# Performance work log

Hardware: AMD Instinct MI355X
Metric: run time of the kernel (lower is better)

Reference implementation:

```python
import jax, jax.numpy as jnp
import numpy as np

HIDDEN = 1024
NUM_HEADS = 16
HEAD_DIM = HIDDEN // NUM_HEADS
WINDOW = 512


def setup_inputs() -> dict:
    key = jax.random.key(0)
    ks = jax.random.split(key, 6)
    b, s = 2, 4096
    x = jax.random.normal(ks[0], (b, s, HIDDEN), dtype=jnp.float32)
    attention_mask = jnp.ones((b, s), dtype=jnp.int32)
    scale = 1.0 / np.sqrt(HIDDEN)
    Wq = jax.random.normal(ks[1], (HIDDEN, HIDDEN), dtype=jnp.float32) * scale
    Wk = jax.random.normal(ks[2], (HIDDEN, HIDDEN), dtype=jnp.float32) * scale
    Wv = jax.random.normal(ks[3], (HIDDEN, HIDDEN), dtype=jnp.float32) * scale
    Wo = jax.random.normal(ks[4], (HIDDEN, HIDDEN), dtype=jnp.float32) * scale
    return {"x": x, "attention_mask": attention_mask,
            "Wq": Wq, "Wk": Wk, "Wv": Wv, "Wo": Wo}


def reference(x, attention_mask, Wq, Wk, Wv, Wo):
    b, s, d = x.shape
    # nn.Linear computes x @ W.T
    q = (x @ Wq.T).reshape(b, s, NUM_HEADS, HEAD_DIM).transpose(0, 2, 1, 3)
    k = (x @ Wk.T).reshape(b, s, NUM_HEADS, HEAD_DIM).transpose(0, 2, 1, 3)
    v = (x @ Wv.T).reshape(b, s, NUM_HEADS, HEAD_DIM).transpose(0, 2, 1, 3)
    # [b,h,s,s] scores
    scores = jnp.einsum('bhqd,bhkd->bhqk', q, k) / np.sqrt(HEAD_DIM)
    # causal sliding-window mask: allow j <= i and j >= i - window + 1
    i = jnp.arange(s)[:, None]
    j = jnp.arange(s)[None, :]
    window_mask = (j <= i) & (j >= i - WINDOW + 1)  # [s,s]
    neg_inf = jnp.finfo(scores.dtype).min
    scores = jnp.where(window_mask[None, None], scores, neg_inf)
    pad = attention_mask.astype(bool)[:, None, None, :]  # [b,1,1,s]
    scores = jnp.where(pad, scores, neg_inf)
    probs = jax.nn.softmax(scores, axis=-1)
    out = jnp.einsum('bhqk,bhkd->bhqd', probs, v)
    out = out.transpose(0, 2, 1, 3).reshape(b, s, d)
    return out @ Wo.T
```

## Files before the change

### kernel.cpp

```cpp
#include <hip/hip_runtime.h>
#include <cstdint>
#include <cstddef>

#define HID 1024
#define SEQ 4096
#define NB  2
#define NH  16
#define HD  64
#define WIN 512
#define TOK (NB*SEQ)

typedef _Float16 f16x8 __attribute__((ext_vector_type(8)));
typedef _Float16 f16x4 __attribute__((ext_vector_type(4)));
typedef float    f32x4 __attribute__((ext_vector_type(4)));

__global__ __launch_bounds__(256)
void convert_kernel(const float* __restrict__ X, const float* __restrict__ w0,
                    const float* __restrict__ w1, const float* __restrict__ w2,
                    const float* __restrict__ w3,
                    _Float16* __restrict__ Xh, _Float16* __restrict__ Wh) {
  const int bi = blockIdx.x;
  const float* src; _Float16* dst; size_t off;
  if (bi < 4096) {
    src = X; dst = Xh; off = (size_t)bi * 2048;
  } else {
    const int wi = bi - 4096, z = wi >> 9;
    src = (z == 0) ? w0 : (z == 1) ? w1 : (z == 2) ? w2 : w3;
    dst = Wh + (size_t)z * HID * HID;
    off = (size_t)(wi & 511) * 2048;
  }
  const size_t i = off + (size_t)threadIdx.x * 8;
  f32x4 a = *(const f32x4*)(src + i);
  f32x4 b = *(const f32x4*)(src + i + 4);
  f16x8 o;
#pragma unroll
  for (int r = 0; r < 4; ++r) { o[r] = (_Float16)a[r]; o[r+4] = (_Float16)b[r]; }
  *(f16x8*)(dst + i) = o;
}

__device__ __forceinline__ void gload16(const void* g, void* lds) {
  __builtin_amdgcn_global_load_lds(
      (__attribute__((address_space(1))) void*)(void*)g,
      (__attribute__((address_space(3))) void*)lds, 16, 0, 0);
}

__device__ __forceinline__ void gemm_mainloop(
    const _Float16* __restrict__ A, const _Float16* __restrict__ W,
    _Float16* sA, _Float16* sB, f32x4 (&acc)[4][4], int m0, int n0) {
  const int tid  = threadIdx.x;
  const int lane = tid & 63;
  const int wave = tid >> 6;
  const int wm = wave >> 1, wn = wave & 1;
  const int l15 = lane & 15, quad = lane >> 4;

  const int o0 = tid * 16;
  const int o1 = o0 + 4096;
  const _Float16* a0 = A + (size_t)(m0 + (o0 >> 6)) * HID + ((o0 & 63) >> 1);
  const _Float16* a1 = A + (size_t)(m0 + (o1 >> 6)) * HID + ((o1 & 63) >> 1);
  const _Float16* w0 = W + (size_t)(n0 + (o0 >> 6)) * HID + ((o0 & 63) >> 1);
  const _Float16* w1 = W + (size_t)(n0 + (o1 >> 6)) * HID + ((o1 & 63) >> 1);
  _Float16* la0 = sA + (o0 >> 1);
  _Float16* la1 = sA + (o1 >> 1);
  _Float16* lb0 = sB + (o0 >> 1);
  _Float16* lb1 = sB + (o1 >> 1);

  const int aoff = (wm*64 + l15)*32 + quad*8;
  const int boff = (wn*64 + l15)*32 + quad*8;

  for (int k0 = 0; k0 < HID; k0 += 64) {
    __syncthreads();
    gload16(a0 + k0,      la0);
    gload16(a1 + k0,      la1);
    gload16(a0 + k0 + 32, la0 + 4096);
    gload16(a1 + k0 + 32, la1 + 4096);
    gload16(w0 + k0,      lb0);
    gload16(w1 + k0,      lb1);
    gload16(w0 + k0 + 32, lb0 + 4096);
    gload16(w1 + k0 + 32, lb1 + 4096);
    __syncthreads();
#pragma unroll
    for (int s = 0; s < 2; ++s) {
      const int sb = s * 4096;
      f16x8 af[4], wf[4];
#pragma unroll
      for (int t = 0; t < 4; ++t) {
        af[t] = *(const f16x8*)(sA + sb + aoff + t*512);
        wf[t] = *(const f16x8*)(sB + sb + boff + t*512);
      }
#pragma unroll
      for (int i = 0; i < 4; ++i)
#pragma unroll
        for (int j = 0; j < 4; ++j)
          acc[i][j] = __builtin_amdgcn_mfma_f32_16x16x32_f16(af[i], wf[j], acc[i][j], 0, 0, 0);
    }
  }
}

__global__ __launch_bounds__(256, 3)
void gemm_qkv_kernel(const _Float16* __restrict__ X,
                     const _Float16* __restrict__ Wh,
                     _Float16* __restrict__ Q,
                     _Float16* __restrict__ Kb,
                     _Float16* __restrict__ Vt) {
  __shared__ __align__(16) _Float16 sA[128*64];
  __shared__ __align__(16) _Float16 sB[128*64];
  const int i  = blockIdx.x;
  const int g  = i & 7;
  const int j  = i >> 3;
  const int mi = j & 7;
  const int c  = j >> 3;
  const int z  = c >> 3;
  const int n0 = (c & 7) * 128;
  const int m0 = (g*8 + mi) * 128;
  const _Float16* W = Wh + (size_t)z * HID * HID;
  f32x4 acc[4][4] = {};
  gemm_mainloop(X, W, sA, sB, acc, m0, n0);

  const int tid  = threadIdx.x;
  const int lane = tid & 63;
  const int wave = tid >> 6;
  const int wm = wave >> 1, wn = wave & 1;
  const int l15 = lane & 15, quad = lane >> 4;

  if (z < 2) {
    _Float16* C = (z == 0) ? Q : Kb;
    const float scl = (z == 0) ? 0.125f : 1.0f;
#pragma unroll
    for (int tm = 0; tm < 4; ++tm)
#pragma unroll
      for (int tn = 0; tn < 4; ++tn) {
        const int row = m0 + wm*64 + tm*16 + quad*4;
        const int col = n0 + wn*64 + tn*16 + l15;
#pragma unroll
        for (int r = 0; r < 4; ++r)
          C[(size_t)(row + r)*HID + col] = (_Float16)(acc[tm][tn][r] * scl);
      }
  } else {
#pragma unroll
    for (int tm = 0; tm < 4; ++tm)
#pragma unroll
      for (int tn = 0; tn < 4; ++tn) {
        const int row = m0 + wm*64 + tm*16 + quad*4;
        const int col = n0 + wn*64 + tn*16 + l15;
        f16x4 v;
#pragma unroll
        for (int r = 0; r < 4; ++r) v[r] = (_Float16)acc[tm][tn][r];
        *(f16x4*)(Vt + (size_t)col*TOK + row) = v;
      }
  }
}

__global__ __launch_bounds__(256, 3)
void gemm_o_kernel(const _Float16* __restrict__ A,
                   const _Float16* __restrict__ Wo,
                   float* __restrict__ C) {
  __shared__ __align__(16) _Float16 sA[128*64];
  __shared__ __align__(16) _Float16 sB[128*64];
  const int i  = blockIdx.x;
  const int g  = i & 7;
  const int j  = i >> 3;
  const int mi = j & 7;
  const int n0 = (j >> 3) * 128;
  const int m0 = (g*8 + mi) * 128;
  f32x4 acc[4][4] = {};
  gemm_mainloop(A, Wo, sA, sB, acc, m0, n0);

  const int tid  = threadIdx.x;
  const int lane = tid & 63;
  const int wave = tid >> 6;
  const int wm = wave >> 1, wn = wave & 1;
  const int l15 = lane & 15, quad = lane >> 4;
#pragma unroll
  for (int tm = 0; tm < 4; ++tm)
#pragma unroll
    for (int tn = 0; tn < 4; ++tn) {
      const int row = m0 + wm*64 + tm*16 + quad*4;
      const int col = n0 + wn*64 + tn*16 + l15;
#pragma unroll
      for (int r = 0; r < 4; ++r)
        C[(size_t)(row + r)*HID + col] = acc[tm][tn][r];
    }
}

__global__ __launch_bounds__(256, 4)
void attn_kernel(const _Float16* __restrict__ Q, const _Float16* __restrict__ Kb,
                 const _Float16* __restrict__ Vt, const int* __restrict__ AM,
                 _Float16* __restrict__ O) {
  __shared__ __align__(16) _Float16 sK[64*64];
  __shared__ __align__(16) _Float16 sV[64*64];
  __shared__ __align__(16) _Float16 sP[4*32*64];
  __shared__ int sOK;

  const int bi = blockIdx.x;
  const int g  = bi & 7;
  const int jj = bi >> 3;
  const int combo = g*4 + (jj >> 5);
  const int h = combo & 15, b = combo >> 4;
  const int qt = jj & 31;

  const int tid  = threadIdx.x;
  const int lane = tid & 63, wave = tid >> 6;
  const int l15 = lane & 15, quad = lane >> 4;

  const int q0 = qt * 128;
  const int qw = q0 + wave * 32;

  const int swz = l15 & 7;
  const int cA8 = ((quad ^ swz) << 3);
  const int cB8 = (((quad + 4) ^ swz) << 3);

  f16x8 qf[2][2];
#pragma unroll
  for (int ns = 0; ns < 2; ++ns) {
    const size_t qb = (size_t)(b*SEQ + qw + ns*16 + l15)*HID + h*HD + quad*8;
    qf[ns][0] = *(const f16x8*)(Q + qb);
    qf[ns][1] = *(const f16x8*)(Q + qb + 32);
  }

  const int kt_hi = 2*qt + 1;
  int kt_lo = 2*qt - 8; if (kt_lo < 0) kt_lo = 0;

  if (tid == 0) sOK = 1;
  __syncthreads();
  {
    int ok = 1;
    const int jbeg = kt_lo*64, jend = (kt_hi + 1)*64;
    for (int j = jbeg + tid; j < jend; j += 256) ok &= (AM[b*SEQ + j] != 0);
    if (!ok) sOK = 0;
  }
  __syncthreads();
  const bool allok = (sOK != 0);

  const int prow = tid >> 3;
  const int pc   = tid & 7;
  const int pco  = ((pc ^ (prow & 7)) << 3);
  f16x8 pk0, pk1, pv0, pv1;
  {
    const int j0 = kt_lo * 64;
    const _Float16* kp = Kb + (size_t)(b*SEQ + j0 + prow)*HID + h*HD + pco;
    pk0 = *(const f16x8*)kp;
    pk1 = *(const f16x8*)(kp + (size_t)32*HID);
    const _Float16* vp = Vt + (size_t)(h*HD + prow)*TOK + b*SEQ + j0 + pco;
    pv0 = *(const f16x8*)vp;
    pv1 = *(const f16x8*)(vp + (size_t)32*TOK);
  }

  float m_run[2] = {-1e20f, -1e20f}, l_run[2] = {0.0f, 0.0f};
  f32x4 o[4][2] = {};
  _Float16* myP = sP + wave * (32*64);

  for (int kt = kt_lo; kt <= kt_hi; ++kt) {
    const int j0 = kt * 64;
    __syncthreads();
    *(f16x8*)(sK + tid*8)        = pk0;
    *(f16x8*)(sK + tid*8 + 2048) = pk1;
    *(f16x8*)(sV + tid*8)        = pv0;
    *(f16x8*)(sV + tid*8 + 2048) = pv1;
    __syncthreads();
    if (kt < kt_hi) {
      int jn = (kt + 1) * 64; if (jn > SEQ - 64) jn = SEQ - 64;
      const _Float16* kp = Kb + (size_t)(b*SEQ + jn + prow)*HID + h*HD + pco;
      pk0 = *(const f16x8*)kp;
      pk1 = *(const f16x8*)(kp + (size_t)32*HID);
      const _Float16* vp = Vt + (size_t)(h*HD + prow)*TOK + b*SEQ + jn + pco;
      pv0 = *(const f16x8*)vp;
      pv1 = *(const f16x8*)(vp + (size_t)32*TOK);
    }

    f32x4 sc[4][2] = {};
#pragma unroll
    for (int t = 0; t < 4; ++t) {
      const f16x8 kf0 = *(const f16x8*)(sK + (t*16 + l15)*64 + cA8);
      const f16x8 kf1 = *(const f16x8*)(sK + (t*16 + l15)*64 + cB8);
      sc[t][0] = __builtin_amdgcn_mfma_f32_16x16x32_f16(kf0, qf[0][0], sc[t][0], 0, 0, 0);
      sc[t][0] = __builtin_amdgcn_mfma_f32_16x16x32_f16(kf1, qf[0][1], sc[t][0], 0, 0, 0);
      sc[t][1] = __builtin_amdgcn_mfma_f32_16x16x32_f16(kf0, qf[1][0], sc[t][1], 0, 0, 0);
      sc[t][1] = __builtin_amdgcn_mfma_f32_16x16x32_f16(kf1, qf[1][1], sc[t][1], 0, 0, 0);
    }

    if (!allok) {
#pragma unroll
      for (int t = 0; t < 4; ++t)
#pragma unroll
        for (int r = 0; r < 4; ++r) {
          const float ad = (AM[b*SEQ + j0 + t*16 + quad*4 + r] == 0) ? -2e30f : 0.0f;
          sc[t][0][r] += ad;
          sc[t][1][r] += ad;
        }
    }

#pragma unroll
    for (int ns = 0; ns < 2; ++ns) {
      const int i = qw + ns*16 + l15;
      float mx = -1e30f;
#pragma unroll
      for (int t = 0; t < 4; ++t)
#pragma unroll
        for (int r = 0; r < 4; ++r) {
          const int j = j0 + t*16 + quad*4 + r;
          const bool valid = (unsigned)(i - j) < WIN;
          const float s = valid ? sc[t][ns][r] : -1e30f;
          sc[t][ns][r] = s;
          mx = fmaxf(mx, s);
        }
      mx = fmaxf(mx, __shfl_xor(mx, 16, 64));
      mx = fmaxf(mx, __shfl_xor(mx, 32, 64));
      const float mnew = fmaxf(m_run[ns], mx);
      const float alpha = __expf(m_run[ns] - mnew);
      m_run[ns] = mnew;
      float sum = 0.0f;
#pragma unroll
      for (int t = 0; t < 4; ++t) {
        f16x4 pv;
#pragma unroll
        for (int r = 0; r < 4; ++r) {
          const float p = __expf(sc[t][ns][r] - mnew);
          sum += p;
          pv[r] = (_Float16)p;
        }
        const int paddr = (ns*16 + l15)*64 + (((2*t + (quad >> 1)) ^ swz) << 3) + (quad & 1)*4;
        *(f16x4*)(myP + paddr) = pv;
      }
      sum += __shfl_xor(sum, 16, 64);
      sum += __shfl_xor(sum, 32, 64);
      l_run[ns] = l_run[ns]*alpha + sum;
#pragma unroll
      for (int dt = 0; dt < 4; ++dt)
#pragma unroll
        for (int r = 0; r < 4; ++r) o[dt][ns][r] *= alpha;
    }

    const f16x8 pf00 = *(const f16x8*)(myP + l15*64 + cA8);
    const f16x8 pf01 = *(const f16x8*)(myP + l15*64 + cB8);
    const f16x8 pf10 = *(const f16x8*)(myP + (16 + l15)*64 + cA8);
    const f16x8 pf11 = *(const f16x8*)(myP + (16 + l15)*64 + cB8);
#pragma unroll
    for (int dt = 0; dt < 4; ++dt) {
      const f16x8 vf0 = *(const f16x8*)(sV + (dt*16 + l15)*64 + cA8);
      const f16x8 vf1 = *(const f16x8*)(sV + (dt*16 + l15)*64 + cB8);
      o[dt][0] = __builtin_amdgcn_mfma_f32_16x16x32_f16(vf0, pf00, o[dt][0], 0, 0, 0);
      o[dt][0] = __builtin_amdgcn_mfma_f32_16x16x32_f16(vf1, pf01, o[dt][0], 0, 0, 0);
      o[dt][1] = __builtin_amdgcn_mfma_f32_16x16x32_f16(vf0, pf10, o[dt][1], 0, 0, 0);
      o[dt][1] = __builtin_amdgcn_mfma_f32_16x16x32_f16(vf1, pf11, o[dt][1], 0, 0, 0);
    }
  }

  const float inv[2] = {1.0f / fmaxf(l_run[0], 1e-30f), 1.0f / fmaxf(l_run[1], 1e-30f)};
#pragma unroll
  for (int ns = 0; ns < 2; ++ns) {
    const size_t ob = (size_t)(b*SEQ + qw + ns*16 + l15)*HID + h*HD + quad*4;
#pragma unroll
    for (int dt = 0; dt < 4; ++dt) {
      f16x4 v;
#pragma unroll
      for (int r = 0; r < 4; ++r) v[r] = (_Float16)(o[dt][ns][r] * inv[ns]);
      *(f16x4*)(O + ob + dt*16) = v;
    }
  }
}

extern "C" void kernel_launch(void* const* d_in, const int* in_sizes, int n_in,
                              void* d_out, int out_size, void* d_ws, size_t ws_size,
                              hipStream_t stream) {
  const float* X  = (const float*)d_in[0];
  const int*   AM = (const int*)d_in[1];
  const float* Wq = (const float*)d_in[2];
  const float* Wk = (const float*)d_in[3];
  const float* Wv = (const float*)d_in[4];
  const float* Wo = (const float*)d_in[5];
  float* out = (float*)d_out;

  _Float16* Xh = (_Float16*)d_ws;
  _Float16* Wh = Xh + (size_t)TOK*HID;
  _Float16* Qb = Wh + (size_t)4*HID*HID;
  _Float16* Kb = Qb + (size_t)TOK*HID;
  _Float16* Vt = Kb + (size_t)TOK*HID;
  _Float16* AO = Vt + (size_t)TOK*HID;

  dim3 blk(256);
  convert_kernel<<<dim3(4096 + 4*512), blk, 0, stream>>>(X, Wq, Wk, Wv, Wo, Xh, Wh);
  gemm_qkv_kernel<<<dim3(1536), blk, 0, stream>>>(Xh, Wh, Qb, Kb, Vt);
  attn_kernel<<<dim3(1024), blk, 0, stream>>>(Qb, Kb, Vt, AM, AO);
  gemm_o_kernel<<<dim3(512), blk, 0, stream>>>(AO, Wh + (size_t)3*HID*HID, out);
}
```

Baseline: 255.8 us.

## Use 256-query attention blocks with 8 waves and skip out-of-window key tiles

The attention kernel now runs 512 threads per block covering 256 queries, so each K/V tile staged in shared memory is reused by twice as many query rows. The grid is halved, and each thread loads a single K/V vector per tile instead of two. Each wave skips MFMA and softmax work for key tiles that fall entirely outside its causal sliding window, since the wider block spans more tiles than any one wave needs. In exchange there are fewer blocks to spread across CUs, the larger block needs more shared memory, and waves sit idle at barriers on skipped tiles.

```diff
diff --git a/kernel.cpp b/kernel.cpp
--- a/kernel.cpp
+++ b/kernel.cpp
@@ -182,27 +182,27 @@
     }
 }
 
-__global__ __launch_bounds__(256, 4)
+__global__ __launch_bounds__(512, 4)
 void attn_kernel(const _Float16* __restrict__ Q, const _Float16* __restrict__ Kb,
                  const _Float16* __restrict__ Vt, const int* __restrict__ AM,
                  _Float16* __restrict__ O) {
   __shared__ __align__(16) _Float16 sK[64*64];
   __shared__ __align__(16) _Float16 sV[64*64];
-  __shared__ __align__(16) _Float16 sP[4*32*64];
+  __shared__ __align__(16) _Float16 sP[8*32*64];
   __shared__ int sOK;
 
   const int bi = blockIdx.x;
   const int g  = bi & 7;
   const int jj = bi >> 3;
-  const int combo = g*4 + (jj >> 5);
+  const int combo = g*4 + (jj >> 4);
   const int h = combo & 15, b = combo >> 4;
-  const int qt = jj & 31;
+  const int qb = jj & 15;
 
   const int tid  = threadIdx.x;
   const int lane = tid & 63, wave = tid >> 6;
   const int l15 = lane & 15, quad = lane >> 4;
 
-  const int q0 = qt * 128;
+  const int q0 = qb * 256;
   const int qw = q0 + wave * 32;
 
   const int swz = l15 & 7;
@@ -212,20 +212,20 @@
   f16x8 qf[2][2];
 #pragma unroll
   for (int ns = 0; ns < 2; ++ns) {
-    const size_t qb = (size_t)(b*SEQ + qw + ns*16 + l15)*HID + h*HD + quad*8;
-    qf[ns][0] = *(const f16x8*)(Q + qb);
-    qf[ns][1] = *(const f16x8*)(Q + qb + 32);
-  }
-
-  const int kt_hi = 2*qt + 1;
-  int kt_lo = 2*qt - 8; if (kt_lo < 0) kt_lo = 0;
+    const size_t qbse = (size_t)(b*SEQ + qw + ns*16 + l15)*HID + h*HD + quad*8;
+    qf[ns][0] = *(const f16x8*)(Q + qbse);
+    qf[ns][1] = *(const f16x8*)(Q + qbse + 32);
+  }
+
+  const int kt_hi = qb*4 + 3;
+  int kt_lo = qb*4 - 8; if (kt_lo < 0) kt_lo = 0;
 
   if (tid == 0) sOK = 1;
   __syncthreads();
   {
     int ok = 1;
     const int jbeg = kt_lo*64, jend = (kt_hi + 1)*64;
-    for (int j = jbeg + tid; j < jend; j += 256) ok &= (AM[b*SEQ + j] != 0);
+    for (int j = jbeg + tid; j < jend; j += 512) ok &= (AM[b*SEQ + j] != 0);
     if (!ok) sOK = 0;
   }
   __syncthreads();
@@ -234,15 +234,11 @@
   const int prow = tid >> 3;
   const int pc   = tid & 7;
   const int pco  = ((pc ^ (prow & 7)) << 3);
-  f16x8 pk0, pk1, pv0, pv1;
+  f16x8 pk, pv;
   {
     const int j0 = kt_lo * 64;
-    const _Float16* kp = Kb + (size_t)(b*SEQ + j0 + prow)*HID + h*HD + pco;
-    pk0 = *(const f16x8*)kp;
-    pk1 = *(const f16x8*)(kp + (size_t)32*HID);
-    const _Float16* vp = Vt + (size_t)(h*HD + prow)*TOK + b*SEQ + j0 + pco;
-    pv0 = *(const f16x8*)vp;
-    pv1 = *(const f16x8*)(vp + (size_t)32*TOK);
+    pk = *(const f16x8*)(Kb + (size_t)(b*SEQ + j0 + prow)*HID + h*HD + pco);
+    pv = *(const f16x8*)(Vt + (size_t)(h*HD + prow)*TOK + b*SEQ + j0 + pco);
   }
 
   float m_run[2] = {-1e20f, -1e20f}, l_run[2] = {0.0f, 0.0f};
@@ -252,20 +248,16 @@
   for (int kt = kt_lo; kt <= kt_hi; ++kt) {
     const int j0 = kt * 64;
     __syncthreads();
-    *(f16x8*)(sK + tid*8)        = pk0;
-    *(f16x8*)(sK + tid*8 + 2048) = pk1;
-    *(f16x8*)(sV + tid*8)        = pv0;
-    *(f16x8*)(sV + tid*8 + 2048) = pv1;
+    *(f16x8*)(sK + tid*8) = pk;
+    *(f16x8*)(sV + tid*8) = pv;
     __syncthreads();
     if (kt < kt_hi) {
-      int jn = (kt + 1) * 64; if (jn > SEQ - 64) jn = SEQ - 64;
-      const _Float16* kp = Kb + (size_t)(b*SEQ + jn + prow)*HID + h*HD + pco;
-      pk0 = *(const f16x8*)kp;
-      pk1 = *(const f16x8*)(kp + (size_t)32*HID);
-      const _Float16* vp = Vt + (size_t)(h*HD + prow)*TOK + b*SEQ + jn + pco;
-      pv0 = *(const f16x8*)vp;
-      pv1 = *(const f16x8*)(vp + (size_t)32*TOK);
-    }
+      const int jn = (kt + 1) * 64;
+      pk = *(const f16x8*)(Kb + (size_t)(b*SEQ + jn + prow)*HID + h*HD + pco);
+      pv = *(const f16x8*)(Vt + (size_t)(h*HD + prow)*TOK + b*SEQ + jn + pco);
+    }
+
+    if (j0 > qw + 31 || j0 + 63 < qw - (WIN - 1)) continue;
 
     f32x4 sc[4][2] = {};
 #pragma unroll
@@ -311,15 +303,15 @@
       float sum = 0.0f;
 #pragma unroll
       for (int t = 0; t < 4; ++t) {
-        f16x4 pv;
+        f16x4 pvv;
 #pragma unroll
         for (int r = 0; r < 4; ++r) {
           const float p = __expf(sc[t][ns][r] - mnew);
           sum += p;
-          pv[r] = (_Float16)p;
+          pvv[r] = (_Float16)p;
         }
         const int paddr = (ns*16 + l15)*64 + (((2*t + (quad >> 1)) ^ swz) << 3) + (quad & 1)*4;
-        *(f16x4*)(myP + paddr) = pv;
+        *(f16x4*)(myP + paddr) = pvv;
       }
       sum += __shfl_xor(sum, 16, 64);
       sum += __shfl_xor(sum, 32, 64);
@@ -377,9 +369,8 @@
   _Float16* Vt = Kb + (size_t)TOK*HID;
   _Float16* AO = Vt + (size_t)TOK*HID;
 
-  dim3 blk(256);
-  convert_kernel<<<dim3(4096 + 4*512), blk, 0, stream>>>(X, Wq, Wk, Wv, Wo, Xh, Wh);
-  gemm_qkv_kernel<<<dim3(1536), blk, 0, stream>>>(Xh, Wh, Qb, Kb, Vt);
-  attn_kernel<<<dim3(1024), blk, 0, stream>>>(Qb, Kb, Vt, AM, AO);
-  gemm_o_kernel<<<dim3(512), blk, 0, stream>>>(AO, Wh + (size_t)3*HID*HID, out);
-}
+  convert_kernel<<<dim3(4096 + 4*512), dim3(256), 0, stream>>>(X, Wq, Wk, Wv, Wo, Xh, Wh);
+  gemm_qkv_kernel<<<dim3(1536), dim3(256), 0, stream>>>(Xh, Wh, Qb, Kb, Vt);
+  attn_kernel<<<dim3(512), dim3(512), 0, stream>>>(Qb, Kb, Vt, AM, AO);
+  gemm_o_kernel<<<dim3(512), dim3(256), 0, stream>>>(AO, Wh + (size_t)3*HID*HID, out);
+}
```

Result: faster. 243.9 us (-4.6%).
